# Kernel optimization log

Measured on AMD Instinct MI355X. Metric: run time of the kernel, lower is better.

Reference implementation:

```python
import jax, jax.numpy as jnp
import numpy as np

N_HEADS = 16
N_KV_HEADS = 4
HEAD_DIM = 128


def setup_inputs() -> dict:
    key = jax.random.key(0)
    ks = jax.random.split(key, 5)
    B, T, C = 4, 2048, 2048
    kv_dim = N_KV_HEADS * HEAD_DIM
    s = 0.02
    return {
        "x": jax.random.normal(ks[0], (B, T, C), jnp.float32),
        "Wq": jax.random.normal(ks[1], (C, C), jnp.float32) * s,
        "Wk": jax.random.normal(ks[2], (kv_dim, C), jnp.float32) * s,
        "Wv": jax.random.normal(ks[3], (kv_dim, C), jnp.float32) * s,
        "Wo": jax.random.normal(ks[4], (C, C), jnp.float32) * s,
    }


def reference(x, Wq, Wk, Wv, Wo):
    B, T, C = x.shape
    n_rep = N_HEADS // N_KV_HEADS
    # projections (nn.Linear: y = x @ W^T), reshape to (B, H, T, D)
    q = (x @ Wq.T).reshape(B, T, N_HEADS, HEAD_DIM).transpose(0, 2, 1, 3)
    k = (x @ Wk.T).reshape(B, T, N_KV_HEADS, HEAD_DIM).transpose(0, 2, 1, 3)
    v = (x @ Wv.T).reshape(B, T, N_KV_HEADS, HEAD_DIM).transpose(0, 2, 1, 3)
    # GQA: expand kv heads (repeat_interleave on head dim)
    k = jnp.repeat(k, n_rep, axis=1)
    v = jnp.repeat(v, n_rep, axis=1)
    scale = 1.0 / np.sqrt(HEAD_DIM).astype(np.float32)
    scores = jnp.einsum("bhqd,bhkd->bhqk", q, k) * scale
    causal = jnp.tril(jnp.ones((T, T), bool))
    scores = jnp.where(causal[None, None], scores, -jnp.inf)
    attn = jax.nn.softmax(scores, axis=-1)  # dropout p=0 -> identity
    out = jnp.einsum("bhqk,bhkd->bhqd", attn, v)
    out = out.transpose(0, 2, 1, 3).reshape(B, T, C)
    return out @ Wo.T
```

## Files before the change

kernel.cpp:

```cpp
#include <hip/hip_runtime.h>

#define TB 4
#define TT 2048
#define TC 2048
#define NH 16
#define NKV 4
#define HD 128
#define KVDIM (NKV*HD)
#define NQKV (TC + 2*KVDIM)
#define MTOK (TB*TT)

typedef __bf16 bf16x8 __attribute__((ext_vector_type(8)));
typedef float  f32x4  __attribute__((ext_vector_type(4)));
typedef float  f32x16 __attribute__((ext_vector_type(16)));
typedef unsigned short ushort_t;
typedef unsigned short us8 __attribute__((ext_vector_type(8)));
typedef unsigned short us4 __attribute__((ext_vector_type(4)));
typedef unsigned int u32x4 __attribute__((ext_vector_type(4)));

#define QSC 0.12751743f

__device__ __forceinline__ ushort_t f2bf(float f) {
    unsigned u = __builtin_bit_cast(unsigned, f);
    u += 0x7fffu + ((u >> 16) & 1u);
    return (ushort_t)(u >> 16);
}

__device__ __forceinline__ void gload16(const ushort_t* g, ushort_t* l) {
    __builtin_amdgcn_global_load_lds(
        (const __attribute__((address_space(1))) unsigned int*)g,
        (__attribute__((address_space(3))) unsigned int*)l, 16, 0, 0);
}

__global__ __launch_bounds__(256) void cast_bf16(const float* __restrict__ in,
                                                 ushort_t* __restrict__ out, long n) {
    long i = (long)blockIdx.x * blockDim.x + threadIdx.x;
    long stride = (long)gridDim.x * blockDim.x;
    for (long e = i * 4; e < n; e += stride * 4) {
        float4 v = *reinterpret_cast<const float4*>(in + e);
        us4 o;
        o[0] = f2bf(v.x); o[1] = f2bf(v.y); o[2] = f2bf(v.z); o[3] = f2bf(v.w);
        *reinterpret_cast<us4*>(out + e) = o;
    }
}

#define LBLK 8192

template<bool OUTF32, bool QSCALE>
__global__ __launch_bounds__(512, 2) void gemm256(const ushort_t* __restrict__ A,
                                                  const ushort_t* __restrict__ Bw,
                                                  float* __restrict__ Cf,
                                                  ushort_t* __restrict__ Cb,
                                                  int M, int N, int Kd, int nbn) {
    extern __shared__ ushort_t lds[];
    const int tid = threadIdx.x;
    const int lane = tid & 63, wid = tid >> 6;
    const int wm = wid >> 2, wn = wid & 3;
    const int g = lane >> 4, l16 = lane & 15;

    const int cpx = gridDim.x >> 3;
    const int swz = (blockIdx.x & 7) * cpx + (blockIdx.x >> 3);
    const int bm = swz / nbn, bn = swz % nbn;

    const ushort_t* Ag = A  + (size_t)bm * 256 * Kd;
    const ushort_t* Bg = Bw + (size_t)bn * 256 * Kd;

    const int r0 = tid >> 3;
    const int p0 = (tid & 7) ^ (r0 & 7);
    const size_t so0 = (size_t)r0 * Kd + p0 * 8;
    const size_t so1 = so0 + (size_t)64 * Kd;
    const int ldsw0 = wid * 512;

    f32x4 acc[8][4] = {};
    bf16x8 aA[4][2], bB[2][2];

    const int NK = Kd >> 6;
    const int NI = Kd >> 7;

#define STAGE(mat, half, tile) do { if ((tile) < NK) {                                   \
    const ushort_t* sg_ = ((mat) ? Bg : Ag) + (size_t)(half) * 128 * Kd + (size_t)(tile) * 64; \
    ushort_t* lb_ = lds + (((((tile)&1)*2 + (mat))*2 + (half)) * LBLK) + ldsw0;          \
    gload16(sg_ + so0, lb_);                                                             \
    gload16(sg_ + so1, lb_ + 4096);                                                      \
} } while(0)

#define LDA(buf, qm) do {                                                                \
    const ushort_t* Ah_ = lds + (((buf)*2 + 0)*2 + wm) * LBLK;                           \
    _Pragma("unroll") for (int mi_ = 0; mi_ < 4; mi_++) {                                \
        const int r_ = (qm)*64 + mi_*16 + l16;                                           \
        _Pragma("unroll") for (int ks_ = 0; ks_ < 2; ks_++)                              \
            aA[mi_][ks_] = *reinterpret_cast<const bf16x8*>(                             \
                Ah_ + r_*64 + (((ks_*4 + g) ^ (r_ & 7)) * 8));                           \
    }                                                                                    \
} while(0)

#define LDB(buf, qn) do {                                                                \
    const ushort_t* Bh_ = lds + (((buf)*2 + 1)*2 + (wn >> 1)) * LBLK;                    \
    _Pragma("unroll") for (int nj_ = 0; nj_ < 2; nj_++) {                                \
        const int r_ = (wn & 1)*64 + (qn)*32 + nj_*16 + l16;                             \
        _Pragma("unroll") for (int ks_ = 0; ks_ < 2; ks_++)                              \
            bB[nj_][ks_] = *reinterpret_cast<const bf16x8*>(                             \
                Bh_ + r_*64 + (((ks_*4 + g) ^ (r_ & 7)) * 8));                           \
    }                                                                                    \
} while(0)

#define MM(qm, qn) do {                                                                  \
    __builtin_amdgcn_s_setprio(1);                                                       \
    _Pragma("unroll") for (int mi_ = 0; mi_ < 4; mi_++)                                  \
    _Pragma("unroll") for (int nj_ = 0; nj_ < 2; nj_++)                                  \
    _Pragma("unroll") for (int ks_ = 0; ks_ < 2; ks_++)                                  \
        acc[(qm)*4 + mi_][(qn)*2 + nj_] = __builtin_amdgcn_mfma_f32_16x16x32_bf16(       \
            aA[mi_][ks_], bB[nj_][ks_], acc[(qm)*4 + mi_][(qn)*2 + nj_], 0, 0, 0);       \
    __builtin_amdgcn_s_setprio(0);                                                       \
} while(0)

#define PH_MID() do {                                                                    \
    __builtin_amdgcn_s_barrier();                                                        \
    asm volatile("s_waitcnt lgkmcnt(0)" ::: "memory");                                   \
    __builtin_amdgcn_sched_barrier(0);                                                   \
} while(0)

#define PH_END() __builtin_amdgcn_s_barrier()
#define PH_END_VM4() do { asm volatile("s_waitcnt vmcnt(4)" ::: "memory");               \
                          __builtin_amdgcn_s_barrier(); } while(0)
#define PH_END_VM0() do { asm volatile("s_waitcnt vmcnt(0)" ::: "memory");               \
                          __builtin_amdgcn_s_barrier(); } while(0)

    STAGE(0, 0, 0); STAGE(0, 1, 0); STAGE(1, 0, 0); STAGE(1, 1, 0);
    STAGE(0, 0, 1); STAGE(0, 1, 1);
    asm volatile("s_waitcnt vmcnt(4)" ::: "memory");
    __builtin_amdgcn_s_barrier();

    for (int i = 0; i < NI; ++i) {
        const int t0 = 2 * i, t1 = 2 * i + 1;
        const bool last = (i == NI - 1);
        LDA(0, 0); LDB(0, 0);
        STAGE(1, 0, t1); STAGE(1, 1, t1);
        PH_MID(); MM(0, 0); PH_END();
        LDB(0, 1);
        PH_MID(); MM(0, 1); PH_END();
        LDA(0, 1); LDB(0, 0);
        PH_MID(); MM(1, 0); PH_END();
        LDB(0, 1);
        STAGE(0, 0, t0 + 2); STAGE(0, 1, t0 + 2);
        PH_MID(); MM(1, 1);
        if (last) PH_END_VM0(); else PH_END_VM4();
        LDA(1, 0); LDB(1, 0);
        STAGE(1, 0, t0 + 2); STAGE(1, 1, t0 + 2);
        PH_MID(); MM(0, 0); PH_END();
        LDB(1, 1);
        PH_MID(); MM(0, 1); PH_END();
        LDA(1, 1); LDB(1, 0);
        PH_MID(); MM(1, 0); PH_END();
        LDB(1, 1);
        STAGE(0, 0, t1 + 2); STAGE(0, 1, t1 + 2);
        PH_MID(); MM(1, 1);
        if (last) PH_END_VM0(); else PH_END_VM4();
    }

#pragma unroll
    for (int mi = 0; mi < 8; mi++)
#pragma unroll
        for (int nj = 0; nj < 4; nj++) {
            const int rbase = bm * 256 + wm * 128 + mi * 16 + g * 4;
            const int col   = bn * 256 + wn * 64 + nj * 16 + l16;
#pragma unroll
            for (int r = 0; r < 4; r++) {
                float v = acc[mi][nj][r];
                if (QSCALE && col < TC) v *= QSC;
                size_t off = (size_t)(rbase + r) * N + col;
                if (OUTF32) Cf[off] = v;
                else        Cb[off] = f2bf(v);
            }
        }
#undef STAGE
#undef LDA
#undef LDB
#undef MM
#undef PH_MID
#undef PH_END
#undef PH_END_VM4
#undef PH_END_VM0
}

#define AQB 128
#define AKB 64
#define NTB (TT/AQB)
#define VTS 72

__global__ __launch_bounds__(256, 2) void attn_kernel(const ushort_t* __restrict__ qkv,
                                                      ushort_t* __restrict__ aout) {
    __shared__ alignas(16) ushort_t Ks[2][AKB * HD];
    __shared__ alignas(16) ushort_t Vt[2][HD * VTS];

    const int tid  = threadIdx.x;
    const int lane = tid & 63, wid = tid >> 6;
    const int hi   = lane >> 5, l31 = lane & 31;
    const int gx   = blockIdx.x;
    const int h    = blockIdx.y;
    const int b    = blockIdx.z;
    const int hk   = h >> 2;
    const size_t rowbase = (size_t)b * TT;

    const ushort_t* kg = qkv + TC + hk * HD;
    const ushort_t* vg = qkv + TC + KVDIM + hk * HD;
    const int rswz = (l31 & 7) << 3;

    us8 sk0, sk1, sk2, sk3;
    unsigned vv2[16];
    const int kr = tid >> 2, dc = (tid & 3) * 32;
    const int vs = ((lane >> 2) & 7) << 3;

    for (int phase = 0; phase < 2; ++phase) {
        const int qb = (phase == 0 ? (NTB - 1 - gx) : gx) * AQB;
        const int q0 = qb + wid * 32;
        const int qrow = q0 + l31;

        bf16x8 qfr[8];
        {
            const ushort_t* qp = qkv + (rowbase + qrow) * NQKV + h * HD + hi * 8;
#pragma unroll
            for (int s = 0; s < 8; s++)
                qfr[s] = *reinterpret_cast<const bf16x8*>(qp + s * 16);
        }

        f32x16 oacc[4];
#pragma unroll
        for (int d = 0; d < 4; d++)
#pragma unroll
            for (int r = 0; r < 16; r++) oacc[d][r] = 0.f;
        float mrun = -1e30f, lsum = 0.f;

        const int ntiles = qb / AKB + 2;

        {
            const ushort_t* ksrc = kg + (rowbase + kr) * NQKV + dc;
            sk0 = *reinterpret_cast<const us8*>(ksrc);
            sk1 = *reinterpret_cast<const us8*>(ksrc + 8);
            sk2 = *reinterpret_cast<const us8*>(ksrc + 16);
            sk3 = *reinterpret_cast<const us8*>(ksrc + 24);
            const ushort_t* vsrc = vg + (rowbase + wid * 16) * NQKV + 2 * lane;
#pragma unroll
            for (int j = 0; j < 16; j++)
                vv2[j] = *reinterpret_cast<const unsigned*>(vsrc + (size_t)j * NQKV);
        }
        if (phase) __syncthreads();

        for (int t = 0; t < ntiles; ++t) {
            const int kp0 = t * AKB;
            const int cur = t & 1;
            {
                const int kb = kr * HD + dc, ksw = (kr & 7) << 3;
                *reinterpret_cast<us8*>(&Ks[cur][(kb     ) ^ ksw]) = sk0;
                *reinterpret_cast<us8*>(&Ks[cur][(kb +  8) ^ ksw]) = sk1;
                *reinterpret_cast<us8*>(&Ks[cur][(kb + 16) ^ ksw]) = sk2;
                *reinterpret_cast<us8*>(&Ks[cur][(kb + 24) ^ ksw]) = sk3;
                u32x4 pl0, pl1, ph0, ph1;
#pragma unroll
                for (int k = 0; k < 4; k++) {
                    unsigned a = vv2[2 * k], c = vv2[2 * k + 1];
                    pl0[k] = (a & 0xffffu) | (c << 16);
                    ph0[k] = (a >> 16) | (c & 0xffff0000u);
                    unsigned a2 = vv2[8 + 2 * k], c2 = vv2[8 + 2 * k + 1];
                    pl1[k] = (a2 & 0xffffu) | (c2 << 16);
                    ph1[k] = (a2 >> 16) | (c2 & 0xffff0000u);
                }
                ushort_t* r0 = &Vt[cur][(2 * lane) * VTS];
                ushort_t* r1 = &Vt[cur][(2 * lane + 1) * VTS];
                const int o0 = (wid * 16) ^ vs, o1 = (wid * 16 + 8) ^ vs;
                *reinterpret_cast<u32x4*>(r0 + o0) = pl0;
                *reinterpret_cast<u32x4*>(r0 + o1) = pl1;
                *reinterpret_cast<u32x4*>(r1 + o0) = ph0;
                *reinterpret_cast<u32x4*>(r1 + o1) = ph1;
            }
            if (t + 1 < ntiles) {
                const int kn = (t + 1) * AKB;
                const ushort_t* ksrc = kg + (rowbase + kn + kr) * NQKV + dc;
                sk0 = *reinterpret_cast<const us8*>(ksrc);
                sk1 = *reinterpret_cast<const us8*>(ksrc + 8);
                sk2 = *reinterpret_cast<const us8*>(ksrc + 16);
                sk3 = *reinterpret_cast<const us8*>(ksrc + 24);
                const ushort_t* vsrc = vg + (rowbase + kn + wid * 16) * NQKV + 2 * lane;
#pragma unroll
                for (int j = 0; j < 16; j++)
                    vv2[j] = *reinterpret_cast<const unsigned*>(vsrc + (size_t)j * NQKV);
            }
            __syncthreads();

            if (kp0 <= q0 + 31) {
                f32x16 s0, s1;
#pragma unroll
                for (int r = 0; r < 16; r++) { s0[r] = 0.f; s1[r] = 0.f; }
                __builtin_amdgcn_s_setprio(1);
#pragma unroll
                for (int ds = 0; ds < 8; ds++) {
                    bf16x8 ka = *reinterpret_cast<const bf16x8*>(
                        &Ks[cur][(l31 * HD + ds * 16 + hi * 8) ^ rswz]);
                    s0 = __builtin_amdgcn_mfma_f32_32x32x16_bf16(ka, qfr[ds], s0, 0, 0, 0);
                }
#pragma unroll
                for (int ds = 0; ds < 8; ds++) {
                    bf16x8 ka = *reinterpret_cast<const bf16x8*>(
                        &Ks[cur][((32 + l31) * HD + ds * 16 + hi * 8) ^ rswz]);
                    s1 = __builtin_amdgcn_mfma_f32_32x32x16_bf16(ka, qfr[ds], s1, 0, 0, 0);
                }
                __builtin_amdgcn_s_setprio(0);
                if (kp0 + 63 > q0) {
#pragma unroll
                    for (int r = 0; r < 16; r++) {
                        int k0i = kp0 + (r & 3) + 8 * (r >> 2) + 4 * hi;
                        if (k0i > qrow)      s0[r] = -1e30f;
                        if (k0i + 32 > qrow) s1[r] = -1e30f;
                    }
                }
                float mx = fmaxf(s0[0], s1[0]);
#pragma unroll
                for (int r = 1; r < 16; r++) mx = fmaxf(mx, fmaxf(s0[r], s1[r]));
                mx = fmaxf(mx, __shfl_xor(mx, 32));
                if (!__all(mx <= mrun + 8.f)) {
                    float mn = fmaxf(mrun, mx);
                    float al = exp2f(mrun - mn);
#pragma unroll
                    for (int d = 0; d < 4; d++)
#pragma unroll
                        for (int r = 0; r < 16; r++) oacc[d][r] *= al;
                    lsum *= al;
                    mrun = mn;
                }
                unsigned pk0[8], pk1[8];
                float ps = 0.f;
#pragma unroll
                for (int w = 0; w < 8; w++) {
                    float a0 = exp2f(s0[2 * w] - mrun), a1 = exp2f(s0[2 * w + 1] - mrun);
                    float b0 = exp2f(s1[2 * w] - mrun), b1 = exp2f(s1[2 * w + 1] - mrun);
                    ps += (a0 + a1) + (b0 + b1);
                    pk0[w] = (unsigned)f2bf(a0) | ((unsigned)f2bf(a1) << 16);
                    pk1[w] = (unsigned)f2bf(b0) | ((unsigned)f2bf(b1) << 16);
                }
                ps += __shfl_xor(ps, 32);
                lsum += ps;
                __builtin_amdgcn_s_setprio(1);
#pragma unroll
                for (int ks = 0; ks < 4; ks++) {
                    const unsigned* pkt = (ks < 2) ? pk0 : pk1;
                    unsigned c00 = pkt[4 * (ks & 1) + 0];
                    unsigned c01 = pkt[4 * (ks & 1) + 1];
                    unsigned c10 = pkt[4 * (ks & 1) + 2];
                    unsigned c11 = pkt[4 * (ks & 1) + 3];
                    unsigned out0 = hi ? c00 : c10;
                    unsigned out1 = hi ? c01 : c11;
                    unsigned rc0 = __shfl_xor(out0, 32);
                    unsigned rc1 = __shfl_xor(out1, 32);
                    u32x4 faw;
                    faw[0] = hi ? rc0 : c00;
                    faw[1] = hi ? rc1 : c01;
                    faw[2] = hi ? c10 : rc0;
                    faw[3] = hi ? c11 : rc1;
                    bf16x8 pa = __builtin_bit_cast(bf16x8, faw);
#pragma unroll
                    for (int dt = 0; dt < 4; dt++) {
                        int doff = dt * 32 + l31;
                        int sr = ((doff >> 3) & 7) << 3;
                        bf16x8 vb = *reinterpret_cast<const bf16x8*>(
                            &Vt[cur][doff * VTS + ((ks * 16 + hi * 8) ^ sr)]);
                        oacc[dt] = __builtin_amdgcn_mfma_f32_32x32x16_bf16(vb, pa, oacc[dt], 0, 0, 0);
                    }
                }
                __builtin_amdgcn_s_setprio(0);
            }
        }

        const float rl = 1.f / lsum;
        ushort_t* orow = aout + (rowbase + qrow) * TC + h * HD;
#pragma unroll
        for (int dt = 0; dt < 4; dt++)
#pragma unroll
            for (int rp = 0; rp < 8; rp++) {
                int d = dt * 32 + ((2 * rp) & 3) + 8 * ((2 * rp) >> 2) + 4 * hi;
                unsigned w = (unsigned)f2bf(oacc[dt][2 * rp] * rl)
                           | ((unsigned)f2bf(oacc[dt][2 * rp + 1] * rl) << 16);
                *reinterpret_cast<unsigned*>(orow + d) = w;
            }
    }
}

extern "C" void kernel_launch(void* const* d_in, const int* in_sizes, int n_in,
                              void* d_out, int out_size, void* d_ws, size_t ws_size,
                              hipStream_t stream) {
    const float* x  = (const float*)d_in[0];
    const float* Wq = (const float*)d_in[1];
    const float* Wk = (const float*)d_in[2];
    const float* Wv = (const float*)d_in[3];
    const float* Wo = (const float*)d_in[4];
    float* out = (float*)d_out;

    ushort_t* x_bf  = (ushort_t*)d_ws;
    ushort_t* wqkv  = x_bf  + (size_t)MTOK * TC;
    ushort_t* wo_bf = wqkv  + (size_t)NQKV * TC;
    ushort_t* qkv   = wo_bf + (size_t)TC * TC;
    ushort_t* attn  = x_bf;

    auto nb = [](long n) { long b = (n / 4 + 255) / 256; return (int)(b > 4096 ? 4096 : b); };

    cast_bf16<<<nb((long)MTOK * TC), 256, 0, stream>>>(x, x_bf, (long)MTOK * TC);
    cast_bf16<<<nb((long)TC * TC),   256, 0, stream>>>(Wq, wqkv, (long)TC * TC);
    cast_bf16<<<nb((long)KVDIM * TC),256, 0, stream>>>(Wk, wqkv + (size_t)TC * TC, (long)KVDIM * TC);
    cast_bf16<<<nb((long)KVDIM * TC),256, 0, stream>>>(Wv, wqkv + (size_t)(TC + KVDIM) * TC, (long)KVDIM * TC);
    cast_bf16<<<nb((long)TC * TC),   256, 0, stream>>>(Wo, wo_bf, (long)TC * TC);

    const int GEMM_LDS = 131072;
    hipFuncSetAttribute(reinterpret_cast<const void*>(gemm256<false, true>),
                        hipFuncAttributeMaxDynamicSharedMemorySize, GEMM_LDS);
    hipFuncSetAttribute(reinterpret_cast<const void*>(gemm256<true, false>),
                        hipFuncAttributeMaxDynamicSharedMemorySize, GEMM_LDS);

    gemm256<false, true><<<dim3(384), 512, GEMM_LDS, stream>>>(
        x_bf, wqkv, nullptr, qkv, MTOK, NQKV, TC, NQKV / 256);

    attn_kernel<<<dim3(NTB / 2, NH, TB), 256, 0, stream>>>(qkv, attn);

    gemm256<true, false><<<dim3(256), 512, GEMM_LDS, stream>>>(
        attn, wo_bf, out, nullptr, MTOK, TC, TC, TC / 256);
}
```

Before: 352.7 us.

## Process paired causal query tiles concurrently in 512-thread attention blocks sharing K/V

```diff
diff --git a/kernel.cpp b/kernel.cpp
--- a/kernel.cpp
+++ b/kernel.cpp
@@ -11,6 +11,7 @@
 #define MTOK (TB*TT)
 
 typedef __bf16 bf16x8 __attribute__((ext_vector_type(8)));
+typedef __bf16 bf16x2 __attribute__((ext_vector_type(2)));
 typedef float  f32x4  __attribute__((ext_vector_type(4)));
 typedef float  f32x16 __attribute__((ext_vector_type(16)));
 typedef unsigned short ushort_t;
@@ -24,6 +25,12 @@
     unsigned u = __builtin_bit_cast(unsigned, f);
     u += 0x7fffu + ((u >> 16) & 1u);
     return (ushort_t)(u >> 16);
+}
+
+__device__ __forceinline__ unsigned pkbf(float lo, float hi) {
+    bf16x2 v;
+    v[0] = (__bf16)lo; v[1] = (__bf16)hi;
+    return __builtin_bit_cast(unsigned, v);
 }
 
 __device__ __forceinline__ void gload16(const ushort_t* g, ushort_t* l) {
@@ -170,7 +177,7 @@
                 if (QSCALE && col < TC) v *= QSC;
                 size_t off = (size_t)(rbase + r) * N + col;
                 if (OUTF32) Cf[off] = v;
-                else        Cb[off] = f2bf(v);
+                else        Cb[off] = __builtin_bit_cast(ushort_t, (__bf16)v);
             }
         }
 #undef STAGE
@@ -188,7 +195,7 @@
 #define NTB (TT/AQB)
 #define VTS 72
 
-__global__ __launch_bounds__(256, 2) void attn_kernel(const ushort_t* __restrict__ qkv,
+__global__ __launch_bounds__(512, 4) void attn_kernel(const ushort_t* __restrict__ qkv,
                                                       ushort_t* __restrict__ aout) {
     __shared__ alignas(16) ushort_t Ks[2][AKB * HD];
     __shared__ alignas(16) ushort_t Vt[2][HD * VTS];
@@ -206,182 +213,164 @@
     const ushort_t* vg = qkv + TC + KVDIM + hk * HD;
     const int rswz = (l31 & 7) << 3;
 
-    us8 sk0, sk1, sk2, sk3;
-    unsigned vv2[16];
-    const int kr = tid >> 2, dc = (tid & 3) * 32;
-    const int vs = ((lane >> 2) & 7) << 3;
-
-    for (int phase = 0; phase < 2; ++phase) {
-        const int qb = (phase == 0 ? (NTB - 1 - gx) : gx) * AQB;
-        const int q0 = qb + wid * 32;
-        const int qrow = q0 + l31;
-
-        bf16x8 qfr[8];
+    const int qb   = (wid < 4 ? (NTB - 1 - gx) : gx) * AQB;
+    const int q0   = qb + (wid & 3) * 32;
+    const int qrow = q0 + l31;
+    const int ntiles = 2 * (NTB - gx);
+
+    bf16x8 qfr[8];
+    {
+        const ushort_t* qp = qkv + (rowbase + qrow) * NQKV + h * HD + hi * 8;
+#pragma unroll
+        for (int s = 0; s < 8; s++)
+            qfr[s] = *reinterpret_cast<const bf16x8*>(qp + s * 16);
+    }
+
+    f32x16 oacc[4];
+#pragma unroll
+    for (int d = 0; d < 4; d++)
+#pragma unroll
+        for (int r = 0; r < 16; r++) oacc[d][r] = 0.f;
+    float mrun = -1e30f, lsum = 0.f;
+
+    const int kr = tid >> 3, dcK = (tid & 7) * 16;
+    const int ksw = (kr & 7) << 3;
+    const int kb0 = kr * HD + dcK;
+    const int vd2 = (tid & 63) * 2;
+    const int vso = ((wid ^ ((lane >> 2) & 7)) * 8);
+    us8 sk0, sk1;
+    unsigned vv[8];
+
+    {
+        const ushort_t* ksrc = kg + (rowbase + kr) * NQKV + dcK;
+        sk0 = *reinterpret_cast<const us8*>(ksrc);
+        sk1 = *reinterpret_cast<const us8*>(ksrc + 8);
+        const ushort_t* vsrc = vg + (rowbase + wid * 8) * NQKV + vd2;
+#pragma unroll
+        for (int j = 0; j < 8; j++)
+            vv[j] = *reinterpret_cast<const unsigned*>(vsrc + (size_t)j * NQKV);
+    }
+
+    for (int t = 0; t < ntiles; ++t) {
+        const int kp0 = t * AKB;
+        const int cur = t & 1;
         {
-            const ushort_t* qp = qkv + (rowbase + qrow) * NQKV + h * HD + hi * 8;
-#pragma unroll
-            for (int s = 0; s < 8; s++)
-                qfr[s] = *reinterpret_cast<const bf16x8*>(qp + s * 16);
+            *reinterpret_cast<us8*>(&Ks[cur][(kb0    ) ^ ksw]) = sk0;
+            *reinterpret_cast<us8*>(&Ks[cur][(kb0 + 8) ^ ksw]) = sk1;
+            u32x4 plo, phi;
+#pragma unroll
+            for (int k = 0; k < 4; k++) {
+                plo[k] = __builtin_amdgcn_perm(vv[2 * k + 1], vv[2 * k], 0x05040100u);
+                phi[k] = __builtin_amdgcn_perm(vv[2 * k + 1], vv[2 * k], 0x07060302u);
+            }
+            *reinterpret_cast<u32x4*>(&Vt[cur][(vd2    ) * VTS + vso]) = plo;
+            *reinterpret_cast<u32x4*>(&Vt[cur][(vd2 + 1) * VTS + vso]) = phi;
         }
-
-        f32x16 oacc[4];
-#pragma unroll
-        for (int d = 0; d < 4; d++)
-#pragma unroll
-            for (int r = 0; r < 16; r++) oacc[d][r] = 0.f;
-        float mrun = -1e30f, lsum = 0.f;
-
-        const int ntiles = qb / AKB + 2;
-
-        {
-            const ushort_t* ksrc = kg + (rowbase + kr) * NQKV + dc;
+        if (t + 1 < ntiles) {
+            const int kn = (t + 1) * AKB;
+            const ushort_t* ksrc = kg + (rowbase + kn + kr) * NQKV + dcK;
             sk0 = *reinterpret_cast<const us8*>(ksrc);
             sk1 = *reinterpret_cast<const us8*>(ksrc + 8);
-            sk2 = *reinterpret_cast<const us8*>(ksrc + 16);
-            sk3 = *reinterpret_cast<const us8*>(ksrc + 24);
-            const ushort_t* vsrc = vg + (rowbase + wid * 16) * NQKV + 2 * lane;
-#pragma unroll
-            for (int j = 0; j < 16; j++)
-                vv2[j] = *reinterpret_cast<const unsigned*>(vsrc + (size_t)j * NQKV);
+            const ushort_t* vsrc = vg + (rowbase + kn + wid * 8) * NQKV + vd2;
+#pragma unroll
+            for (int j = 0; j < 8; j++)
+                vv[j] = *reinterpret_cast<const unsigned*>(vsrc + (size_t)j * NQKV);
         }
-        if (phase) __syncthreads();
-
-        for (int t = 0; t < ntiles; ++t) {
-            const int kp0 = t * AKB;
-            const int cur = t & 1;
-            {
-                const int kb = kr * HD + dc, ksw = (kr & 7) << 3;
-                *reinterpret_cast<us8*>(&Ks[cur][(kb     ) ^ ksw]) = sk0;
-                *reinterpret_cast<us8*>(&Ks[cur][(kb +  8) ^ ksw]) = sk1;
-                *reinterpret_cast<us8*>(&Ks[cur][(kb + 16) ^ ksw]) = sk2;
-                *reinterpret_cast<us8*>(&Ks[cur][(kb + 24) ^ ksw]) = sk3;
-                u32x4 pl0, pl1, ph0, ph1;
-#pragma unroll
-                for (int k = 0; k < 4; k++) {
-                    unsigned a = vv2[2 * k], c = vv2[2 * k + 1];
-                    pl0[k] = (a & 0xffffu) | (c << 16);
-                    ph0[k] = (a >> 16) | (c & 0xffff0000u);
-                    unsigned a2 = vv2[8 + 2 * k], c2 = vv2[8 + 2 * k + 1];
-                    pl1[k] = (a2 & 0xffffu) | (c2 << 16);
-                    ph1[k] = (a2 >> 16) | (c2 & 0xffff0000u);
+        __syncthreads();
+
+        if (kp0 <= q0 + 31) {
+            f32x16 s0, s1;
+#pragma unroll
+            for (int r = 0; r < 16; r++) { s0[r] = 0.f; s1[r] = 0.f; }
+            __builtin_amdgcn_s_setprio(1);
+#pragma unroll
+            for (int ds = 0; ds < 8; ds++) {
+                bf16x8 ka = *reinterpret_cast<const bf16x8*>(
+                    &Ks[cur][(l31 * HD + ds * 16 + hi * 8) ^ rswz]);
+                s0 = __builtin_amdgcn_mfma_f32_32x32x16_bf16(ka, qfr[ds], s0, 0, 0, 0);
+            }
+#pragma unroll
+            for (int ds = 0; ds < 8; ds++) {
+                bf16x8 ka = *reinterpret_cast<const bf16x8*>(
+                    &Ks[cur][((32 + l31) * HD + ds * 16 + hi * 8) ^ rswz]);
+                s1 = __builtin_amdgcn_mfma_f32_32x32x16_bf16(ka, qfr[ds], s1, 0, 0, 0);
+            }
+            __builtin_amdgcn_s_setprio(0);
+            if (kp0 + 63 > q0) {
+#pragma unroll
+                for (int r = 0; r < 16; r++) {
+                    int k0i = kp0 + (r & 3) + 8 * (r >> 2) + 4 * hi;
+                    if (k0i > qrow)      s0[r] = -1e30f;
+                    if (k0i + 32 > qrow) s1[r] = -1e30f;
                 }
-                ushort_t* r0 = &Vt[cur][(2 * lane) * VTS];
-                ushort_t* r1 = &Vt[cur][(2 * lane + 1) * VTS];
-                const int o0 = (wid * 16) ^ vs, o1 = (wid * 16 + 8) ^ vs;
-                *reinterpret_cast<u32x4*>(r0 + o0) = pl0;
-                *reinterpret_cast<u32x4*>(r0 + o1) = pl1;
-                *reinterpret_cast<u32x4*>(r1 + o0) = ph0;
-                *reinterpret_cast<u32x4*>(r1 + o1) = ph1;
-            }
-            if (t + 1 < ntiles) {
-                const int kn = (t + 1) * AKB;
-                const ushort_t* ksrc = kg + (rowbase + kn + kr) * NQKV + dc;
-                sk0 = *reinterpret_cast<const us8*>(ksrc);
-                sk1 = *reinterpret_cast<const us8*>(ksrc + 8);
-                sk2 = *reinterpret_cast<const us8*>(ksrc + 16);
-                sk3 = *reinterpret_cast<const us8*>(ksrc + 24);
-                const ushort_t* vsrc = vg + (rowbase + kn + wid * 16) * NQKV + 2 * lane;
-#pragma unroll
-                for (int j = 0; j < 16; j++)
-                    vv2[j] = *reinterpret_cast<const unsigned*>(vsrc + (size_t)j * NQKV);
-            }
-            __syncthreads();
-
-            if (kp0 <= q0 + 31) {
-                f32x16 s0, s1;
-#pragma unroll
-                for (int r = 0; r < 16; r++) { s0[r] = 0.f; s1[r] = 0.f; }
-                __builtin_amdgcn_s_setprio(1);
-#pragma unroll
-                for (int ds = 0; ds < 8; ds++) {
-                    bf16x8 ka = *reinterpret_cast<const bf16x8*>(
-                        &Ks[cur][(l31 * HD + ds * 16 + hi * 8) ^ rswz]);
-                    s0 = __builtin_amdgcn_mfma_f32_32x32x16_bf16(ka, qfr[ds], s0, 0, 0, 0);
+            }
+            float mx = fmaxf(s0[0], s1[0]);
+#pragma unroll
+            for (int r = 1; r < 16; r++) mx = fmaxf(mx, fmaxf(s0[r], s1[r]));
+            mx = fmaxf(mx, __shfl_xor(mx, 32));
+            if (!__all(mx <= mrun + 8.f)) {
+                float mn = fmaxf(mrun, mx);
+                float al = exp2f(mrun - mn);
+#pragma unroll
+                for (int d = 0; d < 4; d++)
+#pragma unroll
+                    for (int r = 0; r < 16; r++) oacc[d][r] *= al;
+                lsum *= al;
+                mrun = mn;
+            }
+            unsigned pk0[8], pk1[8];
+            float ps = 0.f;
+#pragma unroll
+            for (int w = 0; w < 8; w++) {
+                float a0 = exp2f(s0[2 * w] - mrun), a1 = exp2f(s0[2 * w + 1] - mrun);
+                float b0 = exp2f(s1[2 * w] - mrun), b1 = exp2f(s1[2 * w + 1] - mrun);
+                ps += (a0 + a1) + (b0 + b1);
+                pk0[w] = pkbf(a0, a1);
+                pk1[w] = pkbf(b0, b1);
+            }
+            ps += __shfl_xor(ps, 32);
+            lsum += ps;
+            __builtin_amdgcn_s_setprio(1);
+#pragma unroll
+            for (int ks = 0; ks < 4; ks++) {
+                const unsigned* pkt = (ks < 2) ? pk0 : pk1;
+                unsigned c00 = pkt[4 * (ks & 1) + 0];
+                unsigned c01 = pkt[4 * (ks & 1) + 1];
+                unsigned c10 = pkt[4 * (ks & 1) + 2];
+                unsigned c11 = pkt[4 * (ks & 1) + 3];
+                unsigned out0 = hi ? c00 : c10;
+                unsigned out1 = hi ? c01 : c11;
+                unsigned rc0 = __shfl_xor(out0, 32);
+                unsigned rc1 = __shfl_xor(out1, 32);
+                u32x4 faw;
+                faw[0] = hi ? rc0 : c00;
+                faw[1] = hi ? rc1 : c01;
+                faw[2] = hi ? c10 : rc0;
+                faw[3] = hi ? c11 : rc1;
+                bf16x8 pa = __builtin_bit_cast(bf16x8, faw);
+#pragma unroll
+                for (int dt = 0; dt < 4; dt++) {
+                    int doff = dt * 32 + l31;
+                    int sr = ((doff >> 3) & 7) << 3;
+                    bf16x8 vb = *reinterpret_cast<const bf16x8*>(
+                        &Vt[cur][doff * VTS + ((ks * 16 + hi * 8) ^ sr)]);
+                    oacc[dt] = __builtin_amdgcn_mfma_f32_32x32x16_bf16(vb, pa, oacc[dt], 0, 0, 0);
                 }
-#pragma unroll
-                for (int ds = 0; ds < 8; ds++) {
-                    bf16x8 ka = *reinterpret_cast<const bf16x8*>(
-                        &Ks[cur][((32 + l31) * HD + ds * 16 + hi * 8) ^ rswz]);
-                    s1 = __builtin_amdgcn_mfma_f32_32x32x16_bf16(ka, qfr[ds], s1, 0, 0, 0);
-                }
-                __builtin_amdgcn_s_setprio(0);
-                if (kp0 + 63 > q0) {
-#pragma unroll
-                    for (int r = 0; r < 16; r++) {
-                        int k0i = kp0 + (r & 3) + 8 * (r >> 2) + 4 * hi;
-                        if (k0i > qrow)      s0[r] = -1e30f;
-                        if (k0i + 32 > qrow) s1[r] = -1e30f;
-                    }
-                }
-                float mx = fmaxf(s0[0], s1[0]);
-#pragma unroll
-                for (int r = 1; r < 16; r++) mx = fmaxf(mx, fmaxf(s0[r], s1[r]));
-                mx = fmaxf(mx, __shfl_xor(mx, 32));
-                if (!__all(mx <= mrun + 8.f)) {
-                    float mn = fmaxf(mrun, mx);
-                    float al = exp2f(mrun - mn);
-#pragma unroll
-                    for (int d = 0; d < 4; d++)
-#pragma unroll
-                        for (int r = 0; r < 16; r++) oacc[d][r] *= al;
-                    lsum *= al;
-                    mrun = mn;
-                }
-                unsigned pk0[8], pk1[8];
-                float ps = 0.f;
-#pragma unroll
-                for (int w = 0; w < 8; w++) {
-                    float a0 = exp2f(s0[2 * w] - mrun), a1 = exp2f(s0[2 * w + 1] - mrun);
-                    float b0 = exp2f(s1[2 * w] - mrun), b1 = exp2f(s1[2 * w + 1] - mrun);
-                    ps += (a0 + a1) + (b0 + b1);
-                    pk0[w] = (unsigned)f2bf(a0) | ((unsigned)f2bf(a1) << 16);
-                    pk1[w] = (unsigned)f2bf(b0) | ((unsigned)f2bf(b1) << 16);
-                }
-                ps += __shfl_xor(ps, 32);
-                lsum += ps;
-                __builtin_amdgcn_s_setprio(1);
-#pragma unroll
-                for (int ks = 0; ks < 4; ks++) {
-                    const unsigned* pkt = (ks < 2) ? pk0 : pk1;
-                    unsigned c00 = pkt[4 * (ks & 1) + 0];
-                    unsigned c01 = pkt[4 * (ks & 1) + 1];
-                    unsigned c10 = pkt[4 * (ks & 1) + 2];
-                    unsigned c11 = pkt[4 * (ks & 1) + 3];
-                    unsigned out0 = hi ? c00 : c10;
-                    unsigned out1 = hi ? c01 : c11;
-                    unsigned rc0 = __shfl_xor(out0, 32);
-                    unsigned rc1 = __shfl_xor(out1, 32);
-                    u32x4 faw;
-                    faw[0] = hi ? rc0 : c00;
-                    faw[1] = hi ? rc1 : c01;
-                    faw[2] = hi ? c10 : rc0;
-                    faw[3] = hi ? c11 : rc1;
-                    bf16x8 pa = __builtin_bit_cast(bf16x8, faw);
-#pragma unroll
-                    for (int dt = 0; dt < 4; dt++) {
-                        int doff = dt * 32 + l31;
-                        int sr = ((doff >> 3) & 7) << 3;
-                        bf16x8 vb = *reinterpret_cast<const bf16x8*>(
-                            &Vt[cur][doff * VTS + ((ks * 16 + hi * 8) ^ sr)]);
-                        oacc[dt] = __builtin_amdgcn_mfma_f32_32x32x16_bf16(vb, pa, oacc[dt], 0, 0, 0);
-                    }
-                }
-                __builtin_amdgcn_s_setprio(0);
-            }
+            }
+            __builtin_amdgcn_s_setprio(0);
         }
-
-        const float rl = 1.f / lsum;
-        ushort_t* orow = aout + (rowbase + qrow) * TC + h * HD;
-#pragma unroll
-        for (int dt = 0; dt < 4; dt++)
-#pragma unroll
-            for (int rp = 0; rp < 8; rp++) {
-                int d = dt * 32 + ((2 * rp) & 3) + 8 * ((2 * rp) >> 2) + 4 * hi;
-                unsigned w = (unsigned)f2bf(oacc[dt][2 * rp] * rl)
-                           | ((unsigned)f2bf(oacc[dt][2 * rp + 1] * rl) << 16);
-                *reinterpret_cast<unsigned*>(orow + d) = w;
-            }
     }
+
+    const float rl = 1.f / lsum;
+    ushort_t* orow = aout + (rowbase + qrow) * TC + h * HD;
+#pragma unroll
+    for (int dt = 0; dt < 4; dt++)
+#pragma unroll
+        for (int rp = 0; rp < 8; rp++) {
+            int d = dt * 32 + ((2 * rp) & 3) + 8 * ((2 * rp) >> 2) + 4 * hi;
+            unsigned w = pkbf(oacc[dt][2 * rp] * rl, oacc[dt][2 * rp + 1] * rl);
+            *reinterpret_cast<unsigned*>(orow + d) = w;
+        }
 }
 
 extern "C" void kernel_launch(void* const* d_in, const int* in_sizes, int n_in,
@@ -417,7 +406,7 @@
     gemm256<false, true><<<dim3(384), 512, GEMM_LDS, stream>>>(
         x_bf, wqkv, nullptr, qkv, MTOK, NQKV, TC, NQKV / 256);
 
-    attn_kernel<<<dim3(NTB / 2, NH, TB), 256, 0, stream>>>(qkv, attn);
+    attn_kernel<<<dim3(NTB / 2, NH, TB), 512, 0, stream>>>(qkv, attn);
 
     gemm256<true, false><<<dim3(256), 512, GEMM_LDS, stream>>>(
         attn, wo_bf, out, nullptr, MTOK, TC, TC, TC / 256);
```

Result: slower. 755.7 us (+114.3%).
